# Performance work log

Hardware: AMD Instinct MI355X
Metric: run time of the kernel (lower is better)

Reference implementation:

```python
import jax, jax.numpy as jnp
import numpy as np

N = 50000      # nodes
E = 800000     # edges (before self-loops)
IN_F = 64
HID = 96
OUT_F = 16
L = 16         # num GCN2Conv layers
ALPHA = 0.1
THETA = 0.5


def setup_inputs() -> dict:
    key = jax.random.key(0)
    ks = jax.random.split(key, 6)
    x = jax.random.normal(ks[0], (N, IN_F), jnp.float32)
    edge_index = jax.random.randint(ks[1], (2, E), 0, N, jnp.int64)
    lin0_w = jax.random.normal(ks[2], (HID, IN_F), jnp.float32) * 0.05
    lin0_b = jnp.zeros((HID,), jnp.float32)
    lin1_w = jax.random.normal(ks[3], (OUT_F, HID), jnp.float32) * 0.05
    lin1_b = jnp.zeros((OUT_F,), jnp.float32)
    conv_w = jax.random.normal(ks[4], (L, HID, HID), jnp.float32) * 0.05
    return {"x": x, "edge_index": edge_index, "lin0_w": lin0_w, "lin0_b": lin0_b,
            "lin1_w": lin1_w, "lin1_b": lin1_b, "conv_w": conv_w}


def _gcn_norm(edge_index, n):
    # add self-loops, symmetric normalization D^-1/2 A D^-1/2 (edge weights = 1)
    loops = jnp.arange(n, dtype=edge_index.dtype)
    row = jnp.concatenate([edge_index[0], loops])
    col = jnp.concatenate([edge_index[1], loops])
    ones = jnp.ones(row.shape[0], jnp.float32)
    deg = jax.ops.segment_sum(ones, col, num_segments=n)
    dis = jnp.where(deg > 0, jax.lax.rsqrt(deg), 0.0)
    val = dis[row] * dis[col]
    return row, col, val


def reference(x, edge_index, lin0_w, lin0_b, lin1_w, lin1_b, conv_w):
    n = x.shape[0]
    row, col, val = _gcn_norm(edge_index, n)
    h = jax.nn.relu(x @ lin0_w.T + lin0_b)            # [N, HID]
    x0 = h
    betas = jnp.log(THETA / jnp.arange(1.0, L + 1.0) + 1.0).astype(jnp.float32)

    def layer(h, wb):
        w, beta = wb
        # SpMM: out[i] = sum_{(i,j) in E} val * h[j]
        m = jax.ops.segment_sum(val[:, None] * h[col], row, num_segments=n)
        s = (1.0 - ALPHA) * m + ALPHA * x0            # initial-residual combine
        out = (1.0 - beta) * s + beta * (s @ w)       # identity mapping (shared weights)
        return jax.nn.relu(out), None

    h, _ = jax.lax.scan(layer, h, (conv_w, betas))
    return h @ lin1_w.T + lin1_b
```

## Files before the change

kernel.cpp:

```cpp
#include <hip/hip_runtime.h>

#define NTHREADS 256
#define HID 96
#define INF 64
#define OUTF 16
#define NLAYERS 16
#define NHW 25088
#define CB 128

typedef __attribute__((ext_vector_type(8))) unsigned short ushort8_t;
typedef __attribute__((ext_vector_type(8))) short short8_t;
typedef __attribute__((ext_vector_type(4))) float f32x4_t;

static __device__ __forceinline__ float bf2f(unsigned short u) {
  return __uint_as_float(((unsigned)u) << 16);
}
static __device__ __forceinline__ unsigned short f2bf(float x) {
  unsigned u = __float_as_uint(x);
  return (unsigned short)((u + 0x7FFF + ((u >> 16) & 1)) >> 16);
}
static __device__ __forceinline__ unsigned pack2bf(float a, float b) {
  return (unsigned)f2bf(a) | ((unsigned)f2bf(b) << 16);
}

__global__ __launch_bounds__(NTHREADS) void k_hist(
    const int* __restrict__ idx, int e, unsigned* __restrict__ part, int nw) {
  __shared__ unsigned hh[NHW];
  int tid = threadIdx.x;
  for (int i = tid; i < NHW; i += NTHREADS) hh[i] = 0;
  __syncthreads();
  int per = (e + CB - 1) / CB;
  int s = blockIdx.x * per;
  int en = min(e, s + per);
  for (int i = s + tid; i < en; i += NTHREADS) {
    int v = idx[i];
    atomicAdd(&hh[v >> 1], (v & 1) ? 0x10000u : 1u);
  }
  __syncthreads();
  unsigned* dst = part + (size_t)blockIdx.x * NHW;
  for (int i = tid; i < nw; i += NTHREADS) dst[i] = hh[i];
}

__global__ void k_hmerge(unsigned* __restrict__ partR,
                         const unsigned* __restrict__ partC,
                         int* __restrict__ cnt, float* __restrict__ dis,
                         float* __restrict__ rdis, int n, int nw) {
  int w = blockIdx.x * NTHREADS + threadIdx.x;
  if (w >= nw) return;
  unsigned rl = 0, rh = 0, cl = 0, ch = 0;
#pragma unroll 4
  for (int b = 0; b < CB; ++b) {
    size_t o = (size_t)b * NHW + w;
    unsigned pr = partR[o];
    partR[o] = rl | (rh << 16);
    rl += pr & 0xFFFFu; rh += pr >> 16;
    unsigned pc = partC[o];
    cl += pc & 0xFFFFu; ch += pc >> 16;
  }
  int i0 = 2 * w, i1 = 2 * w + 1;
  if (i0 < n) {
    cnt[i0] = 1 + (int)rl;
    float d = (float)(1 + (int)cl);
    dis[i0] = rsqrtf(d); rdis[i0] = sqrtf(d);
  }
  if (i1 < n) {
    cnt[i1] = 1 + (int)rh;
    float d = (float)(1 + (int)ch);
    dis[i1] = rsqrtf(d); rdis[i1] = sqrtf(d);
  }
}

__global__ void k_scan1(const int* __restrict__ cnt, int* __restrict__ rp,
                        int* __restrict__ bsum, int n) {
  __shared__ int sh[NTHREADS];
  int t = threadIdx.x;
  int i = blockIdx.x * NTHREADS + t;
  int v = (i < n) ? cnt[i] : 0;
  sh[t] = v;
  __syncthreads();
  for (int ofs = 1; ofs < NTHREADS; ofs <<= 1) {
    int u = (t >= ofs) ? sh[t - ofs] : 0;
    __syncthreads();
    sh[t] += u;
    __syncthreads();
  }
  if (i < n) rp[i] = sh[t] - v;
  if (t == NTHREADS - 1) bsum[blockIdx.x] = sh[t];
}

__global__ void k_scan2(int* __restrict__ bsum, int nb) {
  __shared__ int sh[NTHREADS];
  int t = threadIdx.x;
  int v = (t < nb) ? bsum[t] : 0;
  sh[t] = v;
  __syncthreads();
  for (int ofs = 1; ofs < NTHREADS; ofs <<= 1) {
    int u = (t >= ofs) ? sh[t - ofs] : 0;
    __syncthreads();
    sh[t] += u;
    __syncthreads();
  }
  if (t < nb) bsum[t] = sh[t] - v;
}

__global__ void k_scan3(int* __restrict__ rp, const int* __restrict__ bsum,
                        int* __restrict__ ev, int n, int etot) {
  int i = blockIdx.x * NTHREADS + threadIdx.x;
  if (i < n) {
    int v = rp[i] + bsum[blockIdx.x];
    rp[i] = v;
    ev[v] = i;
  }
  if (i == 0) rp[n] = etot;
}

__global__ __launch_bounds__(NTHREADS) void k_scatter3(
    const int* __restrict__ row, const int* __restrict__ col,
    const int* __restrict__ rp, const unsigned* __restrict__ prefR,
    int* __restrict__ ev, int e) {
  __shared__ unsigned lcur[NHW];
  int tid = threadIdx.x;
  for (int i = tid; i < NHW; i += NTHREADS) lcur[i] = 0;
  __syncthreads();
  int per = (e + CB - 1) / CB;
  int s = blockIdx.x * per;
  int en = min(e, s + per);
  const unsigned* pref = prefR + (size_t)blockIdx.x * NHW;
  for (int i = s + tid; i < en; i += NTHREADS) {
    int r = row[i], c = col[i];
    unsigned old = atomicAdd(&lcur[r >> 1], (r & 1) ? 0x10000u : 1u);
    unsigned loc = (r & 1) ? (old >> 16) : (old & 0xFFFFu);
    unsigned pw = pref[r >> 1];
    unsigned pb = (r & 1) ? (pw >> 16) : (pw & 0xFFFFu);
    ev[rp[r] + 1 + (int)pb + (int)loc] = c;
  }
}

__global__ void k_wprime(const float* __restrict__ cw,
                         unsigned short* __restrict__ wTb) {
  int l = blockIdx.y;
  int idx = blockIdx.x * NTHREADS + threadIdx.x;
  int f = idx / HID, k = idx % HID;
  wTb[l * HID * HID + idx] = f2bf(cw[l * HID * HID + k * HID + f]);
}

__global__ __launch_bounds__(NTHREADS) void k_lin0(
    const float* __restrict__ x, const float* __restrict__ w0,
    const float* __restrict__ b0, const float* __restrict__ dis,
    unsigned short* __restrict__ x0b, unsigned short* __restrict__ hs0, int n) {
  __shared__ float wl[INF * HID];
  __shared__ float xT[INF * 68];
  int tid = threadIdx.x;
#pragma unroll
  for (int i = 0; i < 6; ++i) {
    int idx = tid + i * NTHREADS;
    int hrow = idx / 16, q = idx % 16;
    float4 v = *(const float4*)(w0 + hrow * INF + q * 4);
    wl[(q * 4 + 0) * HID + hrow] = v.x;
    wl[(q * 4 + 1) * HID + hrow] = v.y;
    wl[(q * 4 + 2) * HID + hrow] = v.z;
    wl[(q * 4 + 3) * HID + hrow] = v.w;
  }
  int r0 = blockIdx.x * 64;
#pragma unroll
  for (int i = 0; i < 4; ++i) {
    int idx = tid + i * NTHREADS;
    int r = idx / 16, q = idx % 16;
    int gr = r0 + r;
    float4 v = make_float4(0.f, 0.f, 0.f, 0.f);
    if (gr < n) v = *(const float4*)(x + (size_t)gr * INF + q * 4);
    xT[(q * 4 + 0) * 68 + r] = v.x;
    xT[(q * 4 + 1) * 68 + r] = v.y;
    xT[(q * 4 + 2) * 68 + r] = v.z;
    xT[(q * 4 + 3) * 68 + r] = v.w;
  }
  __syncthreads();
  int rg = tid & 15, cg = tid >> 4;
  float acc[4][6];
#pragma unroll
  for (int i = 0; i < 4; ++i)
#pragma unroll
    for (int j = 0; j < 6; ++j) acc[i][j] = 0.f;
#pragma unroll 4
  for (int k = 0; k < INF; ++k) {
    float4 s4 = *(const float4*)(xT + k * 68 + rg * 4);
    const float2* w2 = (const float2*)(wl + k * HID + cg * 6);
    float2 wa = w2[0], wb = w2[1], wc = w2[2];
    float wv[6] = {wa.x, wa.y, wb.x, wb.y, wc.x, wc.y};
    float sv[4] = {s4.x, s4.y, s4.z, s4.w};
#pragma unroll
    for (int i = 0; i < 4; ++i)
#pragma unroll
      for (int j = 0; j < 6; ++j) acc[i][j] = fmaf(sv[i], wv[j], acc[i][j]);
  }
  float bb[6];
#pragma unroll
  for (int j = 0; j < 6; ++j) bb[j] = b0[cg * 6 + j];
#pragma unroll
  for (int i = 0; i < 4; ++i) {
    int gr = r0 + rg * 4 + i;
    if (gr < n) {
      float r_[6];
#pragma unroll
      for (int j = 0; j < 6; ++j) r_[j] = fmaxf(acc[i][j] + bb[j], 0.f);
      float dr = dis[gr];
      unsigned* ob = (unsigned*)(x0b + (size_t)gr * HID + cg * 6);
      ob[0] = pack2bf(r_[0], r_[1]);
      ob[1] = pack2bf(r_[2], r_[3]);
      ob[2] = pack2bf(r_[4], r_[5]);
      unsigned* oh = (unsigned*)(hs0 + (size_t)gr * HID + cg * 6);
      oh[0] = pack2bf(dr * r_[0], dr * r_[1]);
      oh[1] = pack2bf(dr * r_[2], dr * r_[3]);
      oh[2] = pack2bf(dr * r_[4], dr * r_[5]);
    }
  }
}

__global__ __launch_bounds__(NTHREADS) void k_layer(
    const unsigned short* __restrict__ hs, const unsigned short* __restrict__ x0,
    const float* __restrict__ dis, const int* __restrict__ rp,
    const int* __restrict__ ev, const unsigned short* __restrict__ wT,
    unsigned short* __restrict__ hsout, float omb, float beta, int n) {
  __shared__ unsigned char pool[38912] __attribute__((aligned(16)));
  float* red = (float*)pool;
  unsigned short* wl = (unsigned short*)pool;
  unsigned short* sT = (unsigned short*)(pool + 25600);
  int tid = threadIdx.x;
  int hw = tid >> 5, lane = tid & 31;
  int eb = lane >> 2, fg = lane & 3;
  int r0 = blockIdx.x * 64;

  for (int sub = 0; sub < 8; ++sub) {
    int rl = sub * 8 + hw;
    int r = r0 + rl;
    if (r >= n) r = n - 1;
    int e0 = rp[r], e1 = rp[r + 1];
    float acc[24];
#pragma unroll
    for (int j = 0; j < 24; ++j) acc[j] = 0.f;
    int idx0 = e0 + eb;
    bool ok = idx0 < e1;
    idx0 = ok ? idx0 : e1 - 1;
    int cv = ev[idx0];
    for (int base = e0; base < e1; base += 8) {
      int cur = cv;
      bool okc = ok;
      int nb = base + 8;
      if (nb < e1) {
        int i2 = nb + eb;
        ok = i2 < e1;
        i2 = ok ? i2 : e1 - 1;
        cv = ev[i2];
      }
      float v = okc ? 1.f : 0.f;
      const unsigned short* hc = hs + (size_t)cur * HID + fg * 24;
      ushort8_t p0 = *(const ushort8_t*)(hc);
      ushort8_t p1 = *(const ushort8_t*)(hc + 8);
      ushort8_t p2 = *(const ushort8_t*)(hc + 16);
#pragma unroll
      for (int j = 0; j < 8; ++j) acc[j]      = fmaf(v, bf2f(p0[j]), acc[j]);
#pragma unroll
      for (int j = 0; j < 8; ++j) acc[8 + j]  = fmaf(v, bf2f(p1[j]), acc[8 + j]);
#pragma unroll
      for (int j = 0; j < 8; ++j) acc[16 + j] = fmaf(v, bf2f(p2[j]), acc[16 + j]);
    }
    float* myr = red + (hw * 8 + eb) * 100 + fg * 24;
#pragma unroll
    for (int j = 0; j < 6; ++j)
      *(float4*)(myr + j * 4) =
          make_float4(acc[j * 4], acc[j * 4 + 1], acc[j * 4 + 2], acc[j * 4 + 3]);
    asm volatile("s_waitcnt lgkmcnt(0)" ::: "memory");
    __builtin_amdgcn_wave_barrier();
    if (lane < 24) {
      const float* base = red + hw * 800 + lane * 4;
      float4 tot = *(const float4*)(base);
#pragma unroll
      for (int b = 1; b < 8; ++b) {
        float4 p = *(const float4*)(base + b * 100);
        tot.x += p.x; tot.y += p.y; tot.z += p.z; tot.w += p.w;
      }
      float w09 = 0.9f * dis[r];
      const unsigned* xr = (const unsigned*)(x0 + (size_t)r * HID + lane * 4);
      unsigned xa = xr[0], xb = xr[1];
      float s0 = w09 * tot.x + 0.1f * bf2f((unsigned short)(xa & 0xFFFFu));
      float s1 = w09 * tot.y + 0.1f * bf2f((unsigned short)(xa >> 16));
      float s2 = w09 * tot.z + 0.1f * bf2f((unsigned short)(xb & 0xFFFFu));
      float s3 = w09 * tot.w + 0.1f * bf2f((unsigned short)(xb >> 16));
      unsigned* op = (unsigned*)(sT + rl * 104 + lane * 4);
      op[0] = pack2bf(s0, s1);
      op[1] = pack2bf(s2, s3);
    }
    asm volatile("" ::: "memory");
    __builtin_amdgcn_wave_barrier();
  }
  __syncthreads();
#pragma unroll
  for (int i = 0; i < 5; ++i) {
    int idx = tid + i * NTHREADS;
    if (idx < 1152) {
      int f = idx / 12, c = (idx % 12) * 8;
      *(ushort8_t*)(wl + f * 104 + c) = *(const ushort8_t*)(wT + f * HID + c);
    }
  }
  __syncthreads();
  int lane64 = tid & 63, wave = tid >> 6;
  int l15 = lane64 & 15;
  int kg = lane64 >> 4;
  f32x4_t acc2[6];
#pragma unroll
  for (int i = 0; i < 6; ++i) acc2[i] = (f32x4_t)(0.f);
#pragma unroll
  for (int kt = 0; kt < 3; ++kt) {
    short8_t A = *(const short8_t*)(sT + (wave * 16 + l15) * 104 + kt * 32 + kg * 8);
#pragma unroll
    for (int ft = 0; ft < 6; ++ft) {
      short8_t B = *(const short8_t*)(wl + (ft * 16 + l15) * 104 + kt * 32 + kg * 8);
      acc2[ft] = __builtin_amdgcn_mfma_f32_16x16x32_bf16(A, B, acc2[ft], 0, 0, 0);
    }
  }
#pragma unroll
  for (int ft = 0; ft < 6; ++ft) {
    int col = ft * 16 + l15;
#pragma unroll
    for (int j = 0; j < 4; ++j) {
      int rl = wave * 16 + kg * 4 + j;
      int gr = r0 + rl;
      if (gr < n) {
        float sv = bf2f(sT[rl * 104 + col]);
        float o = fmaxf(omb * sv + beta * acc2[ft][j], 0.f);
        hsout[(size_t)gr * HID + col] = f2bf(dis[gr] * o);
      }
    }
  }
}

__global__ __launch_bounds__(NTHREADS) void k_lin1(
    const unsigned short* __restrict__ hs, const float* __restrict__ rdis,
    const float* __restrict__ w1, const float* __restrict__ b1,
    float* __restrict__ out, int n) {
  __shared__ float hT[HID * 68];
  __shared__ float w1l[HID * OUTF];
  int tid = threadIdx.x;
#pragma unroll
  for (int i = 0; i < 6; ++i) {
    int idx = tid + i * NTHREADS;
    int o = idx / HID, k = idx % HID;
    w1l[k * OUTF + o] = w1[idx];
  }
  int r0 = blockIdx.x * 64;
#pragma unroll
  for (int i = 0; i < 3; ++i) {
    int idx = tid + i * NTHREADS;
    int r = idx / 12, q = idx % 12;
    int gr = r0 + r;
    ushort8_t v = (ushort8_t)0;
    float sc = 0.f;
    if (gr < n) {
      v = *(const ushort8_t*)(hs + (size_t)gr * HID + q * 8);
      sc = rdis[gr];
    }
#pragma unroll
    for (int j = 0; j < 8; ++j) hT[(q * 8 + j) * 68 + r] = sc * bf2f(v[j]);
  }
  __syncthreads();
  int r = tid & 63, og = tid >> 6;
  float acc[4] = {0.f, 0.f, 0.f, 0.f};
#pragma unroll 4
  for (int k = 0; k < HID; ++k) {
    float s = hT[k * 68 + r];
    float4 w4 = *(const float4*)(w1l + k * OUTF + og * 4);
    acc[0] = fmaf(s, w4.x, acc[0]);
    acc[1] = fmaf(s, w4.y, acc[1]);
    acc[2] = fmaf(s, w4.z, acc[2]);
    acc[3] = fmaf(s, w4.w, acc[3]);
  }
  int gr = r0 + r;
  if (gr < n) {
    float* op = out + (size_t)gr * OUTF + og * 4;
#pragma unroll
    for (int j = 0; j < 4; ++j) op[j] = acc[j] + b1[og * 4 + j];
  }
}

extern "C" void kernel_launch(void* const* d_in, const int* in_sizes, int n_in,
                              void* d_out, int out_size, void* d_ws, size_t ws_size,
                              hipStream_t stream) {
  const float* x  = (const float*)d_in[0];
  const int*   ei = (const int*)d_in[1];
  const float* w0 = (const float*)d_in[2];
  const float* b0 = (const float*)d_in[3];
  const float* w1 = (const float*)d_in[4];
  const float* b1 = (const float*)d_in[5];
  const float* cw = (const float*)d_in[6];
  int n = in_sizes[0] / INF;
  int e = in_sizes[1] / 2;
  const int* row = ei;
  const int* col = ei + e;

  char* ws = (char*)d_ws;
  size_t off = 0;
  auto alloc = [&](size_t bytes) -> void* {
    void* p = (void*)(ws + off);
    off += (bytes + 255) & ~(size_t)255;
    return p;
  };
  unsigned short* x0b = (unsigned short*)alloc((size_t)n * HID * 2);
  unsigned short* hsA = (unsigned short*)alloc((size_t)n * HID * 2);
  unsigned short* hsB = (unsigned short*)alloc((size_t)n * HID * 2);
  unsigned short* wTb = (unsigned short*)alloc((size_t)NLAYERS * HID * HID * 2);
  float* dis  = (float*)alloc((size_t)n * 4);
  float* rdis = (float*)alloc((size_t)n * 4);
  int*   cnt  = (int*)alloc((size_t)n * 4);
  int*   rp   = (int*)alloc((size_t)(n + 1) * 4);
  int*   ev   = (int*)alloc((size_t)(e + n) * 4);
  int*   bsum = (int*)alloc(1024 * 4);
  unsigned* partR = (unsigned*)x0b;
  unsigned* partC = partR + (size_t)CB * NHW;
  int nw = (n + 1) / 2;
  (void)ws_size; (void)n_in; (void)out_size;

  int nb  = (n + NTHREADS - 1) / NTHREADS;
  int r64 = (n + 63) / 64;

  k_hist<<<CB, NTHREADS, 0, stream>>>(row, e, partR, nw);
  k_hist<<<CB, NTHREADS, 0, stream>>>(col, e, partC, nw);
  k_hmerge<<<(nw + NTHREADS - 1) / NTHREADS, NTHREADS, 0, stream>>>(
      partR, partC, cnt, dis, rdis, n, nw);
  k_scan1<<<nb, NTHREADS, 0, stream>>>(cnt, rp, bsum, n);
  k_scan2<<<1, NTHREADS, 0, stream>>>(bsum, nb);
  k_scan3<<<nb, NTHREADS, 0, stream>>>(rp, bsum, ev, n, e + n);
  k_scatter3<<<CB, NTHREADS, 0, stream>>>(row, col, rp, partR, ev, e);
  k_wprime<<<dim3(36, NLAYERS), NTHREADS, 0, stream>>>(cw, wTb);
  k_lin0<<<r64, NTHREADS, 0, stream>>>(x, w0, b0, dis, x0b, hsA, n);

  const unsigned short* hin = hsA;
  for (int l = 0; l < NLAYERS; ++l) {
    unsigned short* hout = (l & 1) ? hsA : hsB;
    float beta = logf(0.5f / (float)(l + 1) + 1.0f);
    k_layer<<<r64, NTHREADS, 0, stream>>>(hin, x0b, dis, rp, ev,
                                          wTb + (size_t)l * HID * HID, hout,
                                          1.0f - beta, beta, n);
    hin = hout;
  }
  k_lin1<<<r64, NTHREADS, 0, stream>>>(hin, rdis, w1, b1, (float*)d_out, n);
}
```

Baseline: 660.9 us.

## Reduce edge partials with wave shuffles, read weights from global, shrink LDS

Each half-wave's per-row partial sums are now reduced with xor shuffles instead of being written to an LDS scratch area and summed there. The weight tile is read directly from global memory for the MFMA B operand instead of being staged in LDS. That cuts shared memory to only the 64x104 bf16 sT tile. Launch bounds now request higher occupancy to better hide gather latency, but the shuffles add instructions, and indexing acc by the lane-varying eb may force scratch or select chains. The tighter register budget could also cause spills.

```diff
diff --git a/kernel.cpp b/kernel.cpp
--- a/kernel.cpp
+++ b/kernel.cpp
@@ -216,15 +216,12 @@
   }
 }
 
-__global__ __launch_bounds__(NTHREADS) void k_layer(
+__global__ __launch_bounds__(NTHREADS, 8) void k_layer(
     const unsigned short* __restrict__ hs, const unsigned short* __restrict__ x0,
     const float* __restrict__ dis, const int* __restrict__ rp,
     const int* __restrict__ ev, const unsigned short* __restrict__ wT,
     unsigned short* __restrict__ hsout, float omb, float beta, int n) {
-  __shared__ unsigned char pool[38912] __attribute__((aligned(16)));
-  float* red = (float*)pool;
-  unsigned short* wl = (unsigned short*)pool;
-  unsigned short* sT = (unsigned short*)(pool + 25600);
+  __shared__ unsigned short sT[64 * 104];
   int tid = threadIdx.x;
   int hw = tid >> 5, lane = tid & 31;
   int eb = lane >> 2, fg = lane & 3;
@@ -264,42 +261,24 @@
 #pragma unroll
       for (int j = 0; j < 8; ++j) acc[16 + j] = fmaf(v, bf2f(p2[j]), acc[16 + j]);
     }
-    float* myr = red + (hw * 8 + eb) * 100 + fg * 24;
-#pragma unroll
-    for (int j = 0; j < 6; ++j)
-      *(float4*)(myr + j * 4) =
-          make_float4(acc[j * 4], acc[j * 4 + 1], acc[j * 4 + 2], acc[j * 4 + 3]);
-    asm volatile("s_waitcnt lgkmcnt(0)" ::: "memory");
-    __builtin_amdgcn_wave_barrier();
-    if (lane < 24) {
-      const float* base = red + hw * 800 + lane * 4;
-      float4 tot = *(const float4*)(base);
-#pragma unroll
-      for (int b = 1; b < 8; ++b) {
-        float4 p = *(const float4*)(base + b * 100);
-        tot.x += p.x; tot.y += p.y; tot.z += p.z; tot.w += p.w;
-      }
+#pragma unroll
+    for (int j = 0; j < 24; ++j) acc[j] += __shfl_xor(acc[j], 4);
+#pragma unroll
+    for (int j = 0; j < 24; ++j) acc[j] += __shfl_xor(acc[j], 8);
+#pragma unroll
+    for (int j = 0; j < 24; ++j) acc[j] += __shfl_xor(acc[j], 16);
+    if (eb < 6) {
+      int f0 = fg * 24 + eb * 4;
       float w09 = 0.9f * dis[r];
-      const unsigned* xr = (const unsigned*)(x0 + (size_t)r * HID + lane * 4);
+      const unsigned* xr = (const unsigned*)(x0 + (size_t)r * HID + f0);
       unsigned xa = xr[0], xb = xr[1];
-      float s0 = w09 * tot.x + 0.1f * bf2f((unsigned short)(xa & 0xFFFFu));
-      float s1 = w09 * tot.y + 0.1f * bf2f((unsigned short)(xa >> 16));
-      float s2 = w09 * tot.z + 0.1f * bf2f((unsigned short)(xb & 0xFFFFu));
-      float s3 = w09 * tot.w + 0.1f * bf2f((unsigned short)(xb >> 16));
-      unsigned* op = (unsigned*)(sT + rl * 104 + lane * 4);
+      float s0 = w09 * acc[eb * 4 + 0] + 0.1f * bf2f((unsigned short)(xa & 0xFFFFu));
+      float s1 = w09 * acc[eb * 4 + 1] + 0.1f * bf2f((unsigned short)(xa >> 16));
+      float s2 = w09 * acc[eb * 4 + 2] + 0.1f * bf2f((unsigned short)(xb & 0xFFFFu));
+      float s3 = w09 * acc[eb * 4 + 3] + 0.1f * bf2f((unsigned short)(xb >> 16));
+      unsigned* op = (unsigned*)(sT + rl * 104 + f0);
       op[0] = pack2bf(s0, s1);
       op[1] = pack2bf(s2, s3);
-    }
-    asm volatile("" ::: "memory");
-    __builtin_amdgcn_wave_barrier();
-  }
-  __syncthreads();
-#pragma unroll
-  for (int i = 0; i < 5; ++i) {
-    int idx = tid + i * NTHREADS;
-    if (idx < 1152) {
-      int f = idx / 12, c = (idx % 12) * 8;
-      *(ushort8_t*)(wl + f * 104 + c) = *(const ushort8_t*)(wT + f * HID + c);
     }
   }
   __syncthreads();
@@ -314,7 +293,7 @@
     short8_t A = *(const short8_t*)(sT + (wave * 16 + l15) * 104 + kt * 32 + kg * 8);
 #pragma unroll
     for (int ft = 0; ft < 6; ++ft) {
-      short8_t B = *(const short8_t*)(wl + (ft * 16 + l15) * 104 + kt * 32 + kg * 8);
+      short8_t B = *(const short8_t*)(wT + (ft * 16 + l15) * HID + kt * 32 + kg * 8);
       acc2[ft] = __builtin_amdgcn_mfma_f32_16x16x32_bf16(A, B, acc2[ft], 0, 0, 0);
     }
   }
```

Result: slower. 1.330 ms (+101.3%).

## Halve rows per layer block, shuffle-reduce partials, read weights directly from global

Applied to the files above, without the earlier changes.

Each layer block now handles 32 rows instead of 64, and the grid size doubles to match. Edge-partial sums are first combined across lane pairs with a warp shuffle, which halves the shared reduction buffer. The weight matrix is no longer staged in LDS; the MFMA B operands are read straight from global memory, and each wave computes a 16x48 output tile. Together these cut LDS per block and add an occupancy hint, aiming for more resident waves to hide gather latency, at the cost of more global weight reads and less weight reuse per block.

```diff
diff --git a/kernel.cpp b/kernel.cpp
--- a/kernel.cpp
+++ b/kernel.cpp
@@ -216,21 +216,19 @@
   }
 }
 
-__global__ __launch_bounds__(NTHREADS) void k_layer(
+__global__ __launch_bounds__(NTHREADS, 4) void k_layer(
     const unsigned short* __restrict__ hs, const unsigned short* __restrict__ x0,
     const float* __restrict__ dis, const int* __restrict__ rp,
     const int* __restrict__ ev, const unsigned short* __restrict__ wT,
     unsigned short* __restrict__ hsout, float omb, float beta, int n) {
-  __shared__ unsigned char pool[38912] __attribute__((aligned(16)));
-  float* red = (float*)pool;
-  unsigned short* wl = (unsigned short*)pool;
-  unsigned short* sT = (unsigned short*)(pool + 25600);
+  __shared__ float red[8][4][100];
+  __shared__ unsigned short sT[32 * 104];
   int tid = threadIdx.x;
   int hw = tid >> 5, lane = tid & 31;
   int eb = lane >> 2, fg = lane & 3;
-  int r0 = blockIdx.x * 64;
-
-  for (int sub = 0; sub < 8; ++sub) {
+  int r0 = blockIdx.x * 32;
+
+  for (int sub = 0; sub < 4; ++sub) {
     int rl = sub * 8 + hw;
     int r = r0 + rl;
     if (r >= n) r = n - 1;
@@ -264,18 +262,22 @@
 #pragma unroll
       for (int j = 0; j < 8; ++j) acc[16 + j] = fmaf(v, bf2f(p2[j]), acc[16 + j]);
     }
-    float* myr = red + (hw * 8 + eb) * 100 + fg * 24;
-#pragma unroll
-    for (int j = 0; j < 6; ++j)
-      *(float4*)(myr + j * 4) =
-          make_float4(acc[j * 4], acc[j * 4 + 1], acc[j * 4 + 2], acc[j * 4 + 3]);
+#pragma unroll
+    for (int j = 0; j < 24; ++j) acc[j] += __shfl_xor(acc[j], 4);
+    if ((eb & 1) == 0) {
+      float* myr = &red[hw][eb >> 1][fg * 24];
+#pragma unroll
+      for (int j = 0; j < 6; ++j)
+        *(float4*)(myr + j * 4) =
+            make_float4(acc[j * 4], acc[j * 4 + 1], acc[j * 4 + 2], acc[j * 4 + 3]);
+    }
     asm volatile("s_waitcnt lgkmcnt(0)" ::: "memory");
     __builtin_amdgcn_wave_barrier();
     if (lane < 24) {
-      const float* base = red + hw * 800 + lane * 4;
+      const float* base = &red[hw][0][lane * 4];
       float4 tot = *(const float4*)(base);
 #pragma unroll
-      for (int b = 1; b < 8; ++b) {
+      for (int b = 1; b < 4; ++b) {
         float4 p = *(const float4*)(base + b * 100);
         tot.x += p.x; tot.y += p.y; tot.z += p.z; tot.w += p.w;
       }
@@ -294,36 +296,29 @@
     __builtin_amdgcn_wave_barrier();
   }
   __syncthreads();
-#pragma unroll
-  for (int i = 0; i < 5; ++i) {
-    int idx = tid + i * NTHREADS;
-    if (idx < 1152) {
-      int f = idx / 12, c = (idx % 12) * 8;
-      *(ushort8_t*)(wl + f * 104 + c) = *(const ushort8_t*)(wT + f * HID + c);
-    }
-  }
-  __syncthreads();
   int lane64 = tid & 63, wave = tid >> 6;
   int l15 = lane64 & 15;
   int kg = lane64 >> 4;
-  f32x4_t acc2[6];
-#pragma unroll
-  for (int i = 0; i < 6; ++i) acc2[i] = (f32x4_t)(0.f);
+  int rb = (wave & 1) * 16;
+  int cb = (wave >> 1) * 48;
+  f32x4_t acc2[3];
+#pragma unroll
+  for (int i = 0; i < 3; ++i) acc2[i] = (f32x4_t)(0.f);
 #pragma unroll
   for (int kt = 0; kt < 3; ++kt) {
-    short8_t A = *(const short8_t*)(sT + (wave * 16 + l15) * 104 + kt * 32 + kg * 8);
-#pragma unroll
-    for (int ft = 0; ft < 6; ++ft) {
-      short8_t B = *(const short8_t*)(wl + (ft * 16 + l15) * 104 + kt * 32 + kg * 8);
+    short8_t A = *(const short8_t*)(sT + (rb + l15) * 104 + kt * 32 + kg * 8);
+#pragma unroll
+    for (int ft = 0; ft < 3; ++ft) {
+      short8_t B = *(const short8_t*)(wT + (cb + ft * 16 + l15) * HID + kt * 32 + kg * 8);
       acc2[ft] = __builtin_amdgcn_mfma_f32_16x16x32_bf16(A, B, acc2[ft], 0, 0, 0);
     }
   }
 #pragma unroll
-  for (int ft = 0; ft < 6; ++ft) {
-    int col = ft * 16 + l15;
+  for (int ft = 0; ft < 3; ++ft) {
+    int col = cb + ft * 16 + l15;
 #pragma unroll
     for (int j = 0; j < 4; ++j) {
-      int rl = wave * 16 + kg * 4 + j;
+      int rl = rb + kg * 4 + j;
       int gr = r0 + rl;
       if (gr < n) {
         float sv = bf2f(sT[rl * 104 + col]);
@@ -421,6 +416,7 @@
 
   int nb  = (n + NTHREADS - 1) / NTHREADS;
   int r64 = (n + 63) / 64;
+  int r32 = (n + 31) / 32;
 
   k_hist<<<CB, NTHREADS, 0, stream>>>(row, e, partR, nw);
   k_hist<<<CB, NTHREADS, 0, stream>>>(col, e, partC, nw);
@@ -437,7 +433,7 @@
   for (int l = 0; l < NLAYERS; ++l) {
     unsigned short* hout = (l & 1) ? hsA : hsB;
     float beta = logf(0.5f / (float)(l + 1) + 1.0f);
-    k_layer<<<r64, NTHREADS, 0, stream>>>(hin, x0b, dis, rp, ev,
+    k_layer<<<r32, NTHREADS, 0, stream>>>(hin, x0b, dis, rp, ev,
                                           wTb + (size_t)l * HID * HID, hout,
                                           1.0f - beta, beta, n);
     hin = hout;
```

After: 608.0 us, median of 2. -8.0%, faster.
